# Kernel optimization log

Measured on AMD Instinct MI355X. Metric: run time of the kernel, lower is better.

Reference implementation:

```python
import jax, jax.numpy as jnp
import numpy as np

B, N, F = 8, 1024, 256
OUT, REL = 256, 16
NADJ = 7  # ((2 relations + consecutive) * 2 for backward) + self link


def setup_inputs() -> dict:
    key = jax.random.key(0)
    k0, k1, k2, k3, k4 = jax.random.split(key, 5)
    features = jax.random.normal(k0, (B, N, F), dtype=jnp.float32)
    A1 = jax.random.uniform(k1, (B, N, N), dtype=jnp.float32)
    A2 = jax.random.uniform(k2, (B, N, N), dtype=jnp.float32)
    # learned params: one (F+REL, OUT) weight per adjacency matrix, edge embeddings init 'ones', bias (N, OUT)
    W = jax.random.normal(k3, (NADJ, F + REL, OUT), dtype=jnp.float32) * 0.05
    W_edges = jnp.ones((NADJ, REL), dtype=jnp.float32)
    b = jax.random.uniform(k4, (N, OUT), dtype=jnp.float32, minval=-0.05, maxval=0.05)
    return {"features": features, "A1": A1, "A2": A2, "W": W, "W_edges": W_edges, "b": b}


def reference(features, A1, A2, W, W_edges, b):
    # eye = A[0] * zeros(N) + eye(N)  -> batch-broadcast identity [B,N,N]
    eye = jnp.zeros_like(A1) + jnp.eye(N, dtype=A1.dtype)
    # original rolls along axis 0 (batch) of the broadcast identity (faithful replication)
    shifted = jnp.roll(eye, 1, axis=0)
    A_fwd = [A1, A2, shifted]                      # relations + consecutive link
    A_list = A_fwd + [jnp.swapaxes(a, 1, 2) for a in A_fwd]  # backward links
    A_list.append(eye)                             # self links
    A = jnp.stack(A_list, axis=0)                  # [R,B,N,N]

    # concat(features, tile(W_edges[r])) @ W[r] == features @ W[r][:F] + W_edges[r] @ W[r][F:]
    HW = jnp.einsum('bnf,rfo->rbno', features, W[:, :F]) \
         + jnp.einsum('rd,rdo->ro', W_edges, W[:, F:])[:, None, None, :]  # [R,B,N,OUT]
    AHW = jnp.einsum('rbnm,rbmo->rbno', A, HW)     # batched adjacency matmul
    out = jnp.max(AHW, axis=0) + b                 # max-aggregate over relations, add bias
    return out                                     # activation = linear
```

## Files before the change

### kernel.cpp

```cpp
#include <hip/hip_runtime.h>
#include <hip/hip_bf16.h>

#define B_ 8
#define N_ 1024
#define F_ 256
#define OUT_ 256
#define REL_ 16
#define NADJ_ 7

typedef __attribute__((ext_vector_type(8))) _Float16 f16x8;
typedef __attribute__((ext_vector_type(4))) _Float16 f16x4;
typedef __attribute__((ext_vector_type(2))) _Float16 f16x2;
typedef __attribute__((ext_vector_type(4))) float f32x4;

__device__ __forceinline__ void gll16(const _Float16* g, _Float16* l) {
    __builtin_amdgcn_global_load_lds(
        (const __attribute__((address_space(1))) void*)g,
        (__attribute__((address_space(3))) void*)l, 16, 0, 0);
}

__device__ __forceinline__ f16x8 cvt8(float4 a, float4 b) {
    return f16x8{(_Float16)a.x, (_Float16)a.y, (_Float16)a.z, (_Float16)a.w,
                 (_Float16)b.x, (_Float16)b.y, (_Float16)b.z, (_Float16)b.w};
}

__constant__ const int c_perm[7] = {0, 1, 3, 4, 2, 5, 6};

__global__ __launch_bounds__(256) void prep_kernel(const float* __restrict__ W,
                                                   const float* __restrict__ We,
                                                   const float* __restrict__ feat,
                                                   float* __restrict__ cb,
                                                   _Float16* __restrict__ WTp,
                                                   _Float16* __restrict__ Fe) {
    int bid = blockIdx.x, tid = threadIdx.x;
    if (bid < 7) {
        int idx = bid * 256 + tid;
        int j = idx / OUT_, o = idx % OUT_;
        int r = c_perm[j];
        const float* Wr = W + (size_t)r * (F_ + REL_) * OUT_;
        float s = 0.f;
#pragma unroll
        for (int d = 0; d < REL_; ++d) s += We[r * REL_ + d] * Wr[(F_ + d) * OUT_ + o];
        cb[idx] = s;
    } else if (bid < 1799) {
        int idx = (bid - 7) * 256 + tid;
        int j = idx >> 16, rem = idx & 65535, o = rem >> 8, f = rem & 255;
        int r = c_perm[j];
        WTp[idx] = (_Float16)W[((size_t)r * (F_ + REL_) + f) * OUT_ + o];
    } else {
        int i = (bid - 1799) * 256 + tid;
        size_t base = (size_t)i * 8;
        float4 a = *(const float4*)(feat + base);
        float4 b = *(const float4*)(feat + base + 4);
        *(f16x8*)(Fe + base) = cvt8(a, b);
    }
}

__global__ __launch_bounds__(256) void hw7_kernel(const _Float16* __restrict__ Fe,
                                                  const _Float16* __restrict__ WTp,
                                                  const float* __restrict__ cb,
                                                  _Float16* __restrict__ HWT,
                                                  _Float16* __restrict__ HWN) {
    __shared__ _Float16 S[8192];
    const int bid = blockIdx.x, tid = threadIdx.x;
    const int z = bid / 128, rem = bid % 128, bx = rem & 63, by = rem >> 6;
    const bool tr = (z < 4);
    const _Float16* A  = tr ? (WTp + (size_t)z * 65536) : Fe;
    const _Float16* Bt = tr ? Fe : (WTp + (size_t)z * 65536);
    const int m0 = (tr ? by : bx) * 128;
    const int n0 = (tr ? bx : by) * 128;
    _Float16* As = S;
    _Float16* Bs = S + 4096;
    const int wave = tid >> 6, lane = tid & 63, lm = lane & 15, q = lane >> 4;
    const int wr = (wave >> 1) * 64, wc = (wave & 1) * 64;
    const int srow = tid >> 2, sk = (tid & 3) * 8;
    const _Float16* ga0 = A + (size_t)(m0 + srow) * F_ + sk;
    const _Float16* ga1 = ga0 + (size_t)64 * F_;
    const _Float16* gb0 = Bt + (size_t)(n0 + srow) * F_ + sk;
    const _Float16* gb1 = gb0 + (size_t)64 * F_;
    _Float16* la0 = As + tid * 8;
    _Float16* la1 = As + 2048 + tid * 8;
    _Float16* lb0 = Bs + tid * 8;
    _Float16* lb1 = Bs + 2048 + tid * 8;

    f32x4 acc[4][4] = {};
    for (int k0 = 0; k0 < F_; k0 += 32) {
        gll16(ga0 + k0, la0);
        gll16(ga1 + k0, la1);
        gll16(gb0 + k0, lb0);
        gll16(gb1 + k0, lb1);
        __syncthreads();
        f16x8 af[4], bf[4];
#pragma unroll
        for (int i = 0; i < 4; ++i) af[i] = *(const f16x8*)(As + (wr + i * 16 + lm) * 32 + q * 8);
#pragma unroll
        for (int j = 0; j < 4; ++j) bf[j] = *(const f16x8*)(Bs + (wc + j * 16 + lm) * 32 + q * 8);
#pragma unroll
        for (int i = 0; i < 4; ++i)
#pragma unroll
            for (int j = 0; j < 4; ++j)
                acc[i][j] = __builtin_amdgcn_mfma_f32_16x16x32_f16(af[i], bf[j], acc[i][j], 0, 0, 0);
        __syncthreads();
    }
    const float* cbz = cb + (size_t)z * 256;
    if (tr) {
        _Float16* C = HWT + (size_t)z * ((size_t)256 * 8192);
#pragma unroll
        for (int i = 0; i < 4; ++i)
#pragma unroll
            for (int j = 0; j < 4; ++j)
#pragma unroll
                for (int g = 0; g < 4; ++g) {
                    int row = wr + i * 16 + q * 4 + g;
                    int col = wc + j * 16 + lm;
                    float v = acc[i][j][g] + cbz[m0 + row];
                    C[(size_t)(m0 + row) * 8192 + (n0 + col)] = (_Float16)v;
                }
    } else {
        _Float16* C = HWN + (size_t)(z - 4) * ((size_t)8192 * 256);
#pragma unroll
        for (int i = 0; i < 4; ++i)
#pragma unroll
            for (int j = 0; j < 4; ++j)
#pragma unroll
                for (int g = 0; g < 4; ++g) {
                    int row = wr + i * 16 + q * 4 + g;
                    int col = wc + j * 16 + lm;
                    float v = acc[i][j][g] + cbz[n0 + col];
                    C[(size_t)(m0 + row) * 256 + (n0 + col)] = (_Float16)v;
                }
    }
}

__global__ __launch_bounds__(256) void p2_kernel(const float* __restrict__ A1,
                                                 const float* __restrict__ A2,
                                                 const _Float16* __restrict__ HWT,
                                                 _Float16* __restrict__ AHW) {
    __shared__ _Float16 As[2 * 4096];
    __shared__ _Float16 Bs[2 * 4096];
    const int d = blockIdx.x;
    const int xcd = d & 7, slot = d >> 3;
    const int Ghi = xcd + 8 * (slot >> 4);
    const int member = (slot >> 3) & 1;
    const int mt = slot & 7;
    const int kh = Ghi & 1;
    const int zz = Ghi >> 1;
    const int rr = zz >> 3, b = zz & 7;

    const size_t slab = (size_t)B_ * N_ * OUT_;
    const _Float16* Bt = HWT + (size_t)rr * (256 * 8192) + (size_t)b * 1024;
    _Float16* C = AHW + (size_t)kh * (4 * slab) + (size_t)rr * slab + (size_t)b * (N_ * OUT_);
    const int m0 = mt * 128, n0 = member * 128, kbase = kh * 512;
    const int tid = threadIdx.x;
    const int wave = tid >> 6, lane = tid & 63, lm = lane & 15, q = lane >> 4;
    const int wr = (wave >> 1) * 64, wc = (wave & 1) * 64;
    const int srow = tid >> 2, sk = (tid & 3) * 8;
    const _Float16* gb0 = Bt + (size_t)(n0 + srow) * 8192 + kbase + sk;
    const _Float16* gb1 = gb0 + (size_t)64 * 8192;
    _Float16* lb0 = Bs + tid * 8;
    _Float16* lb1 = Bs + 2048 + tid * 8;
    _Float16* la0 = As + srow * 32 + (((tid & 3) ^ ((tid >> 6) & 3)) * 8);

    const float* Ag = ((rr & 1) ? A2 : A1) + (size_t)b * N_ * N_;
    f32x4 acc[4][4] = {};

    auto domfma = [&]() {
#pragma unroll
        for (int u2 = 0; u2 < 2; ++u2) {
            const _Float16* Au = As + u2 * 4096;
            const _Float16* Bu = Bs + u2 * 4096;
            f16x8 af[4], bf[4];
#pragma unroll
            for (int i = 0; i < 4; ++i)
                af[i] = *(const f16x8*)(Au + (wr + i * 16 + lm) * 32 + ((q ^ i) * 8));
#pragma unroll
            for (int j = 0; j < 4; ++j)
                bf[j] = *(const f16x8*)(Bu + (wc + j * 16 + lm) * 32 + q * 8);
#pragma unroll
            for (int i = 0; i < 4; ++i)
#pragma unroll
                for (int j = 0; j < 4; ++j)
                    acc[i][j] = __builtin_amdgcn_mfma_f32_16x16x32_f16(af[i], bf[j], acc[i][j], 0, 0, 0);
        }
    };

    if (rr < 2) {
        const float* Ag0 = Ag + (size_t)(m0 + srow) * N_ + kbase + sk;
        const float* Ag1 = Ag0 + (size_t)64 * N_;
        float4 r0a = *(const float4*)(Ag0);
        float4 r0b = *(const float4*)(Ag0 + 4);
        float4 r1a = *(const float4*)(Ag0 + 32);
        float4 r1b = *(const float4*)(Ag0 + 36);
        float4 r2a = *(const float4*)(Ag1);
        float4 r2b = *(const float4*)(Ag1 + 4);
        float4 r3a = *(const float4*)(Ag1 + 32);
        float4 r3b = *(const float4*)(Ag1 + 36);
        for (int t = 0; t < 8; ++t) {
            gll16(gb0 + t * 64, lb0);
            gll16(gb0 + t * 64 + 32, lb0 + 4096);
            gll16(gb1 + t * 64, lb1);
            gll16(gb1 + t * 64 + 32, lb1 + 4096);
            *(f16x8*)(la0)        = cvt8(r0a, r0b);
            *(f16x8*)(la0 + 4096) = cvt8(r1a, r1b);
            *(f16x8*)(la0 + 2048) = cvt8(r2a, r2b);
            *(f16x8*)(la0 + 6144) = cvt8(r3a, r3b);
            if (t < 7) {
                const float* p0 = Ag0 + (t + 1) * 64;
                const float* p1 = Ag1 + (t + 1) * 64;
                r0a = *(const float4*)(p0);      r0b = *(const float4*)(p0 + 4);
                r1a = *(const float4*)(p0 + 32); r1b = *(const float4*)(p0 + 36);
                r2a = *(const float4*)(p1);      r2b = *(const float4*)(p1 + 4);
                r3a = *(const float4*)(p1 + 32); r3b = *(const float4*)(p1 + 36);
            }
            __syncthreads();
            domfma();
            __syncthreads();
        }
    } else {
        const int kk4 = (tid >> 4) * 4;
        const int ms = (tid & 15) * 8;
        const int u = kk4 >> 5, kl = kk4 & 31;
        const int tsw = ((ms >> 4) & 3) << 3;
        _Float16* wp = As + u * 4096 + ms * 32 + (kl ^ tsw);
        const float* gA = Ag + (size_t)(kbase + kk4) * N_ + m0 + ms;
        float4 ra0 = *(const float4*)(gA);
        float4 rb0 = *(const float4*)(gA + 4);
        float4 ra1 = *(const float4*)(gA + N_);
        float4 rb1 = *(const float4*)(gA + N_ + 4);
        float4 ra2 = *(const float4*)(gA + 2 * N_);
        float4 rb2 = *(const float4*)(gA + 2 * N_ + 4);
        float4 ra3 = *(const float4*)(gA + 3 * N_);
        float4 rb3 = *(const float4*)(gA + 3 * N_ + 4);
        for (int t = 0; t < 8; ++t) {
            gll16(gb0 + t * 64, lb0);
            gll16(gb0 + t * 64 + 32, lb0 + 4096);
            gll16(gb1 + t * 64, lb1);
            gll16(gb1 + t * 64 + 32, lb1 + 4096);
            *(f16x4*)(wp + 0 * 32) = f16x4{(_Float16)ra0.x, (_Float16)ra1.x, (_Float16)ra2.x, (_Float16)ra3.x};
            *(f16x4*)(wp + 1 * 32) = f16x4{(_Float16)ra0.y, (_Float16)ra1.y, (_Float16)ra2.y, (_Float16)ra3.y};
            *(f16x4*)(wp + 2 * 32) = f16x4{(_Float16)ra0.z, (_Float16)ra1.z, (_Float16)ra2.z, (_Float16)ra3.z};
            *(f16x4*)(wp + 3 * 32) = f16x4{(_Float16)ra0.w, (_Float16)ra1.w, (_Float16)ra2.w, (_Float16)ra3.w};
            *(f16x4*)(wp + 4 * 32) = f16x4{(_Float16)rb0.x, (_Float16)rb1.x, (_Float16)rb2.x, (_Float16)rb3.x};
            *(f16x4*)(wp + 5 * 32) = f16x4{(_Float16)rb0.y, (_Float16)rb1.y, (_Float16)rb2.y, (_Float16)rb3.y};
            *(f16x4*)(wp + 6 * 32) = f16x4{(_Float16)rb0.z, (_Float16)rb1.z, (_Float16)rb2.z, (_Float16)rb3.z};
            *(f16x4*)(wp + 7 * 32) = f16x4{(_Float16)rb0.w, (_Float16)rb1.w, (_Float16)rb2.w, (_Float16)rb3.w};
            if (t < 7) {
                const float* p = gA + (size_t)(t + 1) * 64 * N_;
                ra0 = *(const float4*)(p);          rb0 = *(const float4*)(p + 4);
                ra1 = *(const float4*)(p + N_);     rb1 = *(const float4*)(p + N_ + 4);
                ra2 = *(const float4*)(p + 2 * N_); rb2 = *(const float4*)(p + 2 * N_ + 4);
                ra3 = *(const float4*)(p + 3 * N_); rb3 = *(const float4*)(p + 3 * N_ + 4);
            }
            __syncthreads();
            domfma();
            __syncthreads();
        }
    }
#pragma unroll
    for (int i = 0; i < 4; ++i)
#pragma unroll
        for (int j = 0; j < 4; ++j)
#pragma unroll
            for (int g = 0; g < 4; ++g) {
                int row = wr + i * 16 + q * 4 + g;
                int col = wc + j * 16 + lm;
                C[(size_t)(m0 + row) * 256 + (n0 + col)] = (_Float16)acc[i][j][g];
            }
}

__global__ __launch_bounds__(256) void max_kernel(const _Float16* __restrict__ AHW,
                                                  const _Float16* __restrict__ HWN,
                                                  const float* __restrict__ bias,
                                                  float* __restrict__ out) {
    size_t i = ((size_t)blockIdx.x * 256 + threadIdx.x) * 8;
    const size_t slab = (size_t)B_ * N_ * OUT_;
    const size_t HS = 4 * slab;
    float m[8];
    {
        f16x8 v0 = *(const f16x8*)(AHW + i);
        f16x8 v1 = *(const f16x8*)(AHW + HS + i);
#pragma unroll
        for (int e = 0; e < 8; ++e) m[e] = (float)v0[e] + (float)v1[e];
    }
#pragma unroll
    for (int rr = 1; rr < 4; ++rr) {
        f16x8 v0 = *(const f16x8*)(AHW + rr * slab + i);
        f16x8 v1 = *(const f16x8*)(AHW + HS + rr * slab + i);
#pragma unroll
        for (int e = 0; e < 8; ++e) m[e] = fmaxf(m[e], (float)v0[e] + (float)v1[e]);
    }
#pragma unroll
    for (int j = 0; j < 3; ++j) {
        f16x8 w = *(const f16x8*)(HWN + j * slab + i);
#pragma unroll
        for (int e = 0; e < 8; ++e) m[e] = fmaxf(m[e], (float)w[e]);
    }
    size_t bidx = i & ((size_t)N_ * OUT_ - 1);
    float4 b0 = *(const float4*)(bias + bidx);
    float4 b1 = *(const float4*)(bias + bidx + 4);
    float4 o0 = {m[0] + b0.x, m[1] + b0.y, m[2] + b0.z, m[3] + b0.w};
    float4 o1 = {m[4] + b1.x, m[5] + b1.y, m[6] + b1.z, m[7] + b1.w};
    *(float4*)(out + i) = o0;
    *(float4*)(out + i + 4) = o1;
}

__global__ void cbias_kernel(const float* __restrict__ W, const float* __restrict__ We,
                             float* __restrict__ c) {
    int idx = blockIdx.x * 256 + threadIdx.x;
    if (idx >= NADJ_ * OUT_) return;
    int r = idx / OUT_, o = idx % OUT_;
    const float* Wr = W + (size_t)r * (F_ + REL_) * OUT_;
    float s = 0.f;
#pragma unroll
    for (int d = 0; d < REL_; ++d) s += We[r * REL_ + d] * Wr[(F_ + d) * OUT_ + o];
    c[idx] = s;
}

__global__ __launch_bounds__(256) void hw_kernel(const float* __restrict__ feat,
                                                 const float* __restrict__ W,
                                                 const float* __restrict__ cb,
                                                 _Float16* __restrict__ HWb) {
    __shared__ _Float16 As[64][32];
    __shared__ _Float16 Bs[64][32];
    const int mt = blockIdx.x, ct = blockIdx.y;
    const int tid = threadIdx.x, wave = tid >> 6, lane = tid & 63;
    const int r = (ct * 64) / OUT_;
    const int o0 = (ct * 64) % OUT_;
    const float* Bg = W + (size_t)r * (F_ + REL_) * OUT_ + o0;
    const int m0 = mt * 64;
    const int lm = lane & 15, q = lane >> 4;
    f32x4 acc[4] = {};
    for (int k0 = 0; k0 < F_; k0 += 32) {
        {
            int seg = (tid & 3) * 8, m = tid >> 2;
            const float* src = feat + (size_t)(m0 + m) * F_ + k0 + seg;
#pragma unroll
            for (int j = 0; j < 8; ++j) As[m][seg + j] = (_Float16)src[j];
        }
        {
            int kk = tid >> 3, ns = (tid & 7) * 8;
            const float* src = Bg + (size_t)(k0 + kk) * OUT_ + ns;
#pragma unroll
            for (int j = 0; j < 8; ++j) Bs[ns + j][kk] = (_Float16)src[j];
        }
        __syncthreads();
        f16x8 a = *(const f16x8*)&As[wave * 16 + lm][q * 8];
#pragma unroll
        for (int c4 = 0; c4 < 4; ++c4) {
            f16x8 b = *(const f16x8*)&Bs[c4 * 16 + lm][q * 8];
            acc[c4] = __builtin_amdgcn_mfma_f32_16x16x32_f16(a, b, acc[c4], 0, 0, 0);
        }
        __syncthreads();
    }
#pragma unroll
    for (int c4 = 0; c4 < 4; ++c4)
#pragma unroll
        for (int g = 0; g < 4; ++g) {
            int row = wave * 16 + (lane >> 4) * 4 + g;
            int col = c4 * 16 + lm;
            float v = acc[c4][g] + cb[r * OUT_ + o0 + col];
            HWb[((size_t)r * B_ * N_ + m0 + row) * OUT_ + o0 + col] = (_Float16)v;
        }
}

__global__ __launch_bounds__(256) void agg_kernel(const float* __restrict__ A1,
                                                  const float* __restrict__ A2,
                                                  const _Float16* __restrict__ HWb,
                                                  const float* __restrict__ bias,
                                                  float* __restrict__ out) {
    __shared__ _Float16 As[64][32];
    __shared__ _Float16 Bs[64][32];
    const int b = blockIdx.z, nt = blockIdx.y, ot = blockIdx.x;
    const int tid = threadIdx.x, wave = tid >> 6, lane = tid & 63;
    const int n0 = nt * 64, o0 = ot * 64;
    const int lm = lane & 15, q = lane >> 4;
    const size_t rstride = (size_t)B_ * N_ * OUT_;
    f32x4 mx[4];
#pragma unroll
    for (int i = 0; i < 4; ++i) mx[i] = f32x4{-1e30f, -1e30f, -1e30f, -1e30f};
#pragma unroll 1
    for (int rr = 0; rr < 4; ++rr) {
        const float* Ag = ((rr & 1) ? A2 : A1) + (size_t)b * N_ * N_;
        const bool tr = (rr >= 2);
        const int r = (rr < 2) ? rr : rr + 1;
        const _Float16* Bg = HWb + (size_t)r * rstride + (size_t)b * N_ * OUT_ + o0;
        f32x4 acc[4] = {};
        for (int k0 = 0; k0 < N_; k0 += 32) {
            if (!tr) {
                int seg = (tid & 3) * 8, m = tid >> 2;
                const float* src = Ag + (size_t)(n0 + m) * N_ + k0 + seg;
#pragma unroll
                for (int j = 0; j < 8; ++j) As[m][seg + j] = (_Float16)src[j];
            } else {
                int kk = tid >> 3, ms = (tid & 7) * 8;
                const float* src = Ag + (size_t)(k0 + kk) * N_ + n0 + ms;
#pragma unroll
                for (int j = 0; j < 8; ++j) As[ms + j][kk] = (_Float16)src[j];
            }
            {
                int kk = tid >> 3, ns = (tid & 7) * 8;
                const _Float16* src = Bg + (size_t)(k0 + kk) * OUT_ + ns;
#pragma unroll
                for (int j = 0; j < 8; ++j) Bs[ns + j][kk] = src[j];
            }
            __syncthreads();
            f16x8 a = *(const f16x8*)&As[wave * 16 + lm][q * 8];
#pragma unroll
            for (int c4 = 0; c4 < 4; ++c4) {
                f16x8 bb = *(const f16x8*)&Bs[c4 * 16 + lm][q * 8];
                acc[c4] = __builtin_amdgcn_mfma_f32_16x16x32_f16(a, bb, acc[c4], 0, 0, 0);
            }
            __syncthreads();
        }
#pragma unroll
        for (int c4 = 0; c4 < 4; ++c4)
#pragma unroll
            for (int g = 0; g < 4; ++g) mx[c4][g] = fmaxf(mx[c4][g], acc[c4][g]);
    }
#pragma unroll
    for (int c4 = 0; c4 < 4; ++c4)
#pragma unroll
        for (int g = 0; g < 4; ++g) {
            int row = wave * 16 + (lane >> 4) * 4 + g;
            int col = c4 * 16 + lm;
            size_t pos = ((size_t)b * N_ + n0 + row) * OUT_ + o0 + col;
            float v = mx[c4][g];
            v = fmaxf(v, (float)HWb[2 * rstride + pos]);
            v = fmaxf(v, (float)HWb[5 * rstride + pos]);
            v = fmaxf(v, (float)HWb[6 * rstride + pos]);
            out[pos] = v + bias[((size_t)(n0 + row)) * OUT_ + o0 + col];
        }
}

extern "C" void kernel_launch(void* const* d_in, const int* in_sizes, int n_in,
                              void* d_out, int out_size, void* d_ws, size_t ws_size,
                              hipStream_t stream) {
    const float* feat = (const float*)d_in[0];
    const float* A1   = (const float*)d_in[1];
    const float* A2   = (const float*)d_in[2];
    const float* W    = (const float*)d_in[3];
    const float* We   = (const float*)d_in[4];
    const float* bias = (const float*)d_in[5];
    float* out = (float*)d_out;

    const size_t OFF_CB   = 0;
    const size_t OFF_WT   = 8192;
    const size_t OFF_FE   = 1048576;
    const size_t OFF_HWT  = 5242880;
    const size_t OFF_HWN  = 22020096;
    const size_t OFF_AHW  = 34603008;
    const size_t WS_NEEDED = 68157440;

    if (ws_size >= WS_NEEDED) {
        float*    cbp = (float*)((char*)d_ws + OFF_CB);
        _Float16* WTp = (_Float16*)((char*)d_ws + OFF_WT);
        _Float16* Fe  = (_Float16*)((char*)d_ws + OFF_FE);
        _Float16* HWT = (_Float16*)((char*)d_ws + OFF_HWT);
        _Float16* HWN = (_Float16*)((char*)d_ws + OFF_HWN);
        _Float16* AHW = (_Float16*)((char*)d_ws + OFF_AHW);

        prep_kernel<<<2823, 256, 0, stream>>>(W, We, feat, cbp, WTp, Fe);
        hw7_kernel<<<896, 256, 0, stream>>>(Fe, WTp, cbp, HWT, HWN);
        p2_kernel<<<1024, 256, 0, stream>>>(A1, A2, HWT, AHW);
        max_kernel<<<1024, 256, 0, stream>>>(AHW, HWN, bias, out);
    } else {
        float* cb = (float*)d_ws;
        _Float16* HWb = (_Float16*)((char*)d_ws + 8192);
        cbias_kernel<<<7, 256, 0, stream>>>(W, We, cb);
        hw_kernel<<<dim3(128, 28), 256, 0, stream>>>(feat, W, cb, HWb);
        agg_kernel<<<dim3(4, 16, 8), 256, 0, stream>>>(A1, A2, HWb, bias, out);
    }
}
```

Baseline: 174.5 us.

## Double-buffer LDS in GEMM kernels and fuse max over direct relations

```diff
diff --git a/kernel.cpp b/kernel.cpp
--- a/kernel.cpp
+++ b/kernel.cpp
@@ -10,7 +10,6 @@
 
 typedef __attribute__((ext_vector_type(8))) _Float16 f16x8;
 typedef __attribute__((ext_vector_type(4))) _Float16 f16x4;
-typedef __attribute__((ext_vector_type(2))) _Float16 f16x2;
 typedef __attribute__((ext_vector_type(4))) float f32x4;
 
 __device__ __forceinline__ void gll16(const _Float16* g, _Float16* l) {
@@ -60,50 +59,57 @@
                                                   const _Float16* __restrict__ WTp,
                                                   const float* __restrict__ cb,
                                                   _Float16* __restrict__ HWT,
-                                                  _Float16* __restrict__ HWN) {
-    __shared__ _Float16 S[8192];
+                                                  _Float16* __restrict__ HWNm) {
+    __shared__ _Float16 S[2 * 8192];
     const int bid = blockIdx.x, tid = threadIdx.x;
-    const int z = bid / 128, rem = bid % 128, bx = rem & 63, by = rem >> 6;
-    const bool tr = (z < 4);
-    const _Float16* A  = tr ? (WTp + (size_t)z * 65536) : Fe;
-    const _Float16* Bt = tr ? Fe : (WTp + (size_t)z * 65536);
-    const int m0 = (tr ? by : bx) * 128;
-    const int n0 = (tr ? bx : by) * 128;
-    _Float16* As = S;
-    _Float16* Bs = S + 4096;
     const int wave = tid >> 6, lane = tid & 63, lm = lane & 15, q = lane >> 4;
     const int wr = (wave >> 1) * 64, wc = (wave & 1) * 64;
     const int srow = tid >> 2, sk = (tid & 3) * 8;
-    const _Float16* ga0 = A + (size_t)(m0 + srow) * F_ + sk;
-    const _Float16* ga1 = ga0 + (size_t)64 * F_;
-    const _Float16* gb0 = Bt + (size_t)(n0 + srow) * F_ + sk;
-    const _Float16* gb1 = gb0 + (size_t)64 * F_;
-    _Float16* la0 = As + tid * 8;
-    _Float16* la1 = As + 2048 + tid * 8;
-    _Float16* lb0 = Bs + tid * 8;
-    _Float16* lb1 = Bs + 2048 + tid * 8;
 
     f32x4 acc[4][4] = {};
-    for (int k0 = 0; k0 < F_; k0 += 32) {
-        gll16(ga0 + k0, la0);
-        gll16(ga1 + k0, la1);
-        gll16(gb0 + k0, lb0);
-        gll16(gb1 + k0, lb1);
-        __syncthreads();
+
+    auto mfma_step = [&](const _Float16* Au, const _Float16* Bu) {
         f16x8 af[4], bf[4];
 #pragma unroll
-        for (int i = 0; i < 4; ++i) af[i] = *(const f16x8*)(As + (wr + i * 16 + lm) * 32 + q * 8);
-#pragma unroll
-        for (int j = 0; j < 4; ++j) bf[j] = *(const f16x8*)(Bs + (wc + j * 16 + lm) * 32 + q * 8);
+        for (int i = 0; i < 4; ++i) af[i] = *(const f16x8*)(Au + (wr + i * 16 + lm) * 32 + q * 8);
+#pragma unroll
+        for (int j = 0; j < 4; ++j) bf[j] = *(const f16x8*)(Bu + (wc + j * 16 + lm) * 32 + q * 8);
 #pragma unroll
         for (int i = 0; i < 4; ++i)
 #pragma unroll
             for (int j = 0; j < 4; ++j)
                 acc[i][j] = __builtin_amdgcn_mfma_f32_16x16x32_f16(af[i], bf[j], acc[i][j], 0, 0, 0);
+    };
+
+    if (bid < 512) {
+        const int z = bid >> 7, rem = bid & 127, bx = rem & 63, by = rem >> 6;
+        const _Float16* A  = WTp + (size_t)z * 65536;
+        const _Float16* Bt = Fe;
+        const int m0 = by * 128;
+        const int n0 = bx * 128;
+        const _Float16* ga0 = A + (size_t)(m0 + srow) * F_ + sk;
+        const _Float16* ga1 = ga0 + (size_t)64 * F_;
+        const _Float16* gb0 = Bt + (size_t)(n0 + srow) * F_ + sk;
+        const _Float16* gb1 = gb0 + (size_t)64 * F_;
+        gll16(ga0, S + tid * 8);
+        gll16(ga1, S + 2048 + tid * 8);
+        gll16(gb0, S + 4096 + tid * 8);
+        gll16(gb1, S + 6144 + tid * 8);
         __syncthreads();
-    }
-    const float* cbz = cb + (size_t)z * 256;
-    if (tr) {
+        for (int t = 0; t < 8; ++t) {
+            const int c = t & 1, n = c ^ 1;
+            if (t < 7) {
+                const int k = (t + 1) * 32;
+                _Float16* base = S + n * 8192;
+                gll16(ga0 + k, base + tid * 8);
+                gll16(ga1 + k, base + 2048 + tid * 8);
+                gll16(gb0 + k, base + 4096 + tid * 8);
+                gll16(gb1 + k, base + 6144 + tid * 8);
+            }
+            mfma_step(S + c * 8192, S + c * 8192 + 4096);
+            __syncthreads();
+        }
+        const float* cbz = cb + (size_t)z * 256;
         _Float16* C = HWT + (size_t)z * ((size_t)256 * 8192);
 #pragma unroll
         for (int i = 0; i < 4; ++i)
@@ -117,7 +123,55 @@
                     C[(size_t)(m0 + row) * 8192 + (n0 + col)] = (_Float16)v;
                 }
     } else {
-        _Float16* C = HWN + (size_t)(z - 4) * ((size_t)8192 * 256);
+        const int idx = bid - 512, bx = idx & 63, by = idx >> 6;
+        const int m0 = bx * 128;
+        const int n0 = by * 128;
+        const _Float16* ga0 = Fe + (size_t)(m0 + srow) * F_ + sk;
+        const _Float16* ga1 = ga0 + (size_t)64 * F_;
+        float mx[4][4][4];
+#pragma unroll
+        for (int i = 0; i < 4; ++i)
+#pragma unroll
+            for (int j = 0; j < 4; ++j)
+#pragma unroll
+                for (int g = 0; g < 4; ++g) mx[i][j][g] = -1e30f;
+#pragma unroll 1
+        for (int zi = 4; zi < 7; ++zi) {
+            const _Float16* gb0 = WTp + (size_t)zi * 65536 + (size_t)(n0 + srow) * F_ + sk;
+            const _Float16* gb1 = gb0 + (size_t)64 * F_;
+#pragma unroll
+            for (int i = 0; i < 4; ++i)
+#pragma unroll
+                for (int j = 0; j < 4; ++j) acc[i][j] = f32x4{0.f, 0.f, 0.f, 0.f};
+            gll16(ga0, S + tid * 8);
+            gll16(ga1, S + 2048 + tid * 8);
+            gll16(gb0, S + 4096 + tid * 8);
+            gll16(gb1, S + 6144 + tid * 8);
+            __syncthreads();
+            for (int t = 0; t < 8; ++t) {
+                const int c = t & 1, n = c ^ 1;
+                if (t < 7) {
+                    const int k = (t + 1) * 32;
+                    _Float16* base = S + n * 8192;
+                    gll16(ga0 + k, base + tid * 8);
+                    gll16(ga1 + k, base + 2048 + tid * 8);
+                    gll16(gb0 + k, base + 4096 + tid * 8);
+                    gll16(gb1 + k, base + 6144 + tid * 8);
+                }
+                mfma_step(S + c * 8192, S + c * 8192 + 4096);
+                __syncthreads();
+            }
+            const float* cbz = cb + (size_t)zi * 256;
+#pragma unroll
+            for (int i = 0; i < 4; ++i)
+#pragma unroll
+                for (int j = 0; j < 4; ++j)
+#pragma unroll
+                    for (int g = 0; g < 4; ++g) {
+                        int col = wc + j * 16 + lm;
+                        mx[i][j][g] = fmaxf(mx[i][j][g], acc[i][j][g] + cbz[n0 + col]);
+                    }
+        }
 #pragma unroll
         for (int i = 0; i < 4; ++i)
 #pragma unroll
@@ -126,8 +180,7 @@
                 for (int g = 0; g < 4; ++g) {
                     int row = wr + i * 16 + q * 4 + g;
                     int col = wc + j * 16 + lm;
-                    float v = acc[i][j][g] + cbz[n0 + col];
-                    C[(size_t)(m0 + row) * 256 + (n0 + col)] = (_Float16)v;
+                    HWNm[(size_t)(m0 + row) * 256 + (n0 + col)] = (_Float16)mx[i][j][g];
                 }
     }
 }
@@ -157,102 +210,105 @@
     const int srow = tid >> 2, sk = (tid & 3) * 8;
     const _Float16* gb0 = Bt + (size_t)(n0 + srow) * 8192 + kbase + sk;
     const _Float16* gb1 = gb0 + (size_t)64 * 8192;
-    _Float16* lb0 = Bs + tid * 8;
-    _Float16* lb1 = Bs + 2048 + tid * 8;
-    _Float16* la0 = As + srow * 32 + (((tid & 3) ^ ((tid >> 6) & 3)) * 8);
 
     const float* Ag = ((rr & 1) ? A2 : A1) + (size_t)b * N_ * N_;
     f32x4 acc[4][4] = {};
 
-    auto domfma = [&]() {
-#pragma unroll
-        for (int u2 = 0; u2 < 2; ++u2) {
-            const _Float16* Au = As + u2 * 4096;
-            const _Float16* Bu = Bs + u2 * 4096;
-            f16x8 af[4], bf[4];
-#pragma unroll
-            for (int i = 0; i < 4; ++i)
-                af[i] = *(const f16x8*)(Au + (wr + i * 16 + lm) * 32 + ((q ^ i) * 8));
+    auto mfma_step = [&](int c) {
+        const _Float16* Au = As + c * 4096;
+        const _Float16* Bu = Bs + c * 4096;
+        f16x8 af[4], bf[4];
+#pragma unroll
+        for (int i = 0; i < 4; ++i)
+            af[i] = *(const f16x8*)(Au + (wr + i * 16 + lm) * 32 + ((q ^ i) * 8));
+#pragma unroll
+        for (int j = 0; j < 4; ++j)
+            bf[j] = *(const f16x8*)(Bu + (wc + j * 16 + lm) * 32 + q * 8);
+#pragma unroll
+        for (int i = 0; i < 4; ++i)
 #pragma unroll
             for (int j = 0; j < 4; ++j)
-                bf[j] = *(const f16x8*)(Bu + (wc + j * 16 + lm) * 32 + q * 8);
-#pragma unroll
-            for (int i = 0; i < 4; ++i)
-#pragma unroll
-                for (int j = 0; j < 4; ++j)
-                    acc[i][j] = __builtin_amdgcn_mfma_f32_16x16x32_f16(af[i], bf[j], acc[i][j], 0, 0, 0);
-        }
+                acc[i][j] = __builtin_amdgcn_mfma_f32_16x16x32_f16(af[i], bf[j], acc[i][j], 0, 0, 0);
     };
 
     if (rr < 2) {
         const float* Ag0 = Ag + (size_t)(m0 + srow) * N_ + kbase + sk;
         const float* Ag1 = Ag0 + (size_t)64 * N_;
-        float4 r0a = *(const float4*)(Ag0);
-        float4 r0b = *(const float4*)(Ag0 + 4);
-        float4 r1a = *(const float4*)(Ag0 + 32);
-        float4 r1b = *(const float4*)(Ag0 + 36);
-        float4 r2a = *(const float4*)(Ag1);
-        float4 r2b = *(const float4*)(Ag1 + 4);
-        float4 r3a = *(const float4*)(Ag1 + 32);
-        float4 r3b = *(const float4*)(Ag1 + 36);
-        for (int t = 0; t < 8; ++t) {
-            gll16(gb0 + t * 64, lb0);
-            gll16(gb0 + t * 64 + 32, lb0 + 4096);
-            gll16(gb1 + t * 64, lb1);
-            gll16(gb1 + t * 64 + 32, lb1 + 4096);
-            *(f16x8*)(la0)        = cvt8(r0a, r0b);
-            *(f16x8*)(la0 + 4096) = cvt8(r1a, r1b);
-            *(f16x8*)(la0 + 2048) = cvt8(r2a, r2b);
-            *(f16x8*)(la0 + 6144) = cvt8(r3a, r3b);
-            if (t < 7) {
-                const float* p0 = Ag0 + (t + 1) * 64;
-                const float* p1 = Ag1 + (t + 1) * 64;
-                r0a = *(const float4*)(p0);      r0b = *(const float4*)(p0 + 4);
-                r1a = *(const float4*)(p0 + 32); r1b = *(const float4*)(p0 + 36);
-                r2a = *(const float4*)(p1);      r2b = *(const float4*)(p1 + 4);
-                r3a = *(const float4*)(p1 + 32); r3b = *(const float4*)(p1 + 36);
-            }
+        const int sx = ((tid & 3) ^ ((tid >> 6) & 3)) * 8;
+        float4 pa = *(const float4*)(Ag0);
+        float4 pb = *(const float4*)(Ag0 + 4);
+        float4 pc = *(const float4*)(Ag1);
+        float4 pd = *(const float4*)(Ag1 + 4);
+        *(f16x8*)(As + srow * 32 + sx) = cvt8(pa, pb);
+        *(f16x8*)(As + 2048 + srow * 32 + sx) = cvt8(pc, pd);
+        gll16(gb0, Bs + tid * 8);
+        gll16(gb1, Bs + 2048 + tid * 8);
+        pa = *(const float4*)(Ag0 + 32); pb = *(const float4*)(Ag0 + 36);
+        pc = *(const float4*)(Ag1 + 32); pd = *(const float4*)(Ag1 + 36);
+        __syncthreads();
+        for (int t = 0; t < 16; ++t) {
+            const int c = t & 1, n = c ^ 1;
+            if (t < 15) {
+                _Float16* la = As + n * 4096 + srow * 32 + sx;
+                *(f16x8*)(la) = cvt8(pa, pb);
+                *(f16x8*)(la + 2048) = cvt8(pc, pd);
+                gll16(gb0 + (t + 1) * 32, Bs + n * 4096 + tid * 8);
+                gll16(gb1 + (t + 1) * 32, Bs + n * 4096 + 2048 + tid * 8);
+                if (t < 14) {
+                    const int k = (t + 2) * 32;
+                    pa = *(const float4*)(Ag0 + k); pb = *(const float4*)(Ag0 + k + 4);
+                    pc = *(const float4*)(Ag1 + k); pd = *(const float4*)(Ag1 + k + 4);
+                }
+            }
+            mfma_step(c);
             __syncthreads();
-            domfma();
-            __syncthreads();
         }
     } else {
-        const int kk4 = (tid >> 4) * 4;
-        const int ms = (tid & 15) * 8;
-        const int u = kk4 >> 5, kl = kk4 & 31;
-        const int tsw = ((ms >> 4) & 3) << 3;
-        _Float16* wp = As + u * 4096 + ms * 32 + (kl ^ tsw);
-        const float* gA = Ag + (size_t)(kbase + kk4) * N_ + m0 + ms;
+        const int kk4 = (tid >> 5) * 4;
+        const int ms4 = (tid & 31) * 4;
+        const int tsw = ((ms4 >> 4) & 3) << 3;
+        const int wof = ms4 * 32 + (kk4 ^ tsw);
+        const float* gA = Ag + (size_t)(kbase + kk4) * N_ + m0 + ms4;
         float4 ra0 = *(const float4*)(gA);
-        float4 rb0 = *(const float4*)(gA + 4);
         float4 ra1 = *(const float4*)(gA + N_);
-        float4 rb1 = *(const float4*)(gA + N_ + 4);
         float4 ra2 = *(const float4*)(gA + 2 * N_);
-        float4 rb2 = *(const float4*)(gA + 2 * N_ + 4);
         float4 ra3 = *(const float4*)(gA + 3 * N_);
-        float4 rb3 = *(const float4*)(gA + 3 * N_ + 4);
-        for (int t = 0; t < 8; ++t) {
-            gll16(gb0 + t * 64, lb0);
-            gll16(gb0 + t * 64 + 32, lb0 + 4096);
-            gll16(gb1 + t * 64, lb1);
-            gll16(gb1 + t * 64 + 32, lb1 + 4096);
+        {
+            _Float16* wp = As + wof;
             *(f16x4*)(wp + 0 * 32) = f16x4{(_Float16)ra0.x, (_Float16)ra1.x, (_Float16)ra2.x, (_Float16)ra3.x};
             *(f16x4*)(wp + 1 * 32) = f16x4{(_Float16)ra0.y, (_Float16)ra1.y, (_Float16)ra2.y, (_Float16)ra3.y};
             *(f16x4*)(wp + 2 * 32) = f16x4{(_Float16)ra0.z, (_Float16)ra1.z, (_Float16)ra2.z, (_Float16)ra3.z};
             *(f16x4*)(wp + 3 * 32) = f16x4{(_Float16)ra0.w, (_Float16)ra1.w, (_Float16)ra2.w, (_Float16)ra3.w};
-            *(f16x4*)(wp + 4 * 32) = f16x4{(_Float16)rb0.x, (_Float16)rb1.x, (_Float16)rb2.x, (_Float16)rb3.x};
-            *(f16x4*)(wp + 5 * 32) = f16x4{(_Float16)rb0.y, (_Float16)rb1.y, (_Float16)rb2.y, (_Float16)rb3.y};
-            *(f16x4*)(wp + 6 * 32) = f16x4{(_Float16)rb0.z, (_Float16)rb1.z, (_Float16)rb2.z, (_Float16)rb3.z};
-            *(f16x4*)(wp + 7 * 32) = f16x4{(_Float16)rb0.w, (_Float16)rb1.w, (_Float16)rb2.w, (_Float16)rb3.w};
-            if (t < 7) {
-                const float* p = gA + (size_t)(t + 1) * 64 * N_;
-                ra0 = *(const float4*)(p);          rb0 = *(const float4*)(p + 4);
-                ra1 = *(const float4*)(p + N_);     rb1 = *(const float4*)(p + N_ + 4);
-                ra2 = *(const float4*)(p + 2 * N_); rb2 = *(const float4*)(p + 2 * N_ + 4);
-                ra3 = *(const float4*)(p + 3 * N_); rb3 = *(const float4*)(p + 3 * N_ + 4);
-            }
-            __syncthreads();
-            domfma();
+        }
+        gll16(gb0, Bs + tid * 8);
+        gll16(gb1, Bs + 2048 + tid * 8);
+        {
+            const float* p = gA + (size_t)32 * N_;
+            ra0 = *(const float4*)(p);
+            ra1 = *(const float4*)(p + N_);
+            ra2 = *(const float4*)(p + 2 * N_);
+            ra3 = *(const float4*)(p + 3 * N_);
+        }
+        __syncthreads();
+        for (int t = 0; t < 16; ++t) {
+            const int c = t & 1, n = c ^ 1;
+            if (t < 15) {
+                _Float16* wp = As + n * 4096 + wof;
+                *(f16x4*)(wp + 0 * 32) = f16x4{(_Float16)ra0.x, (_Float16)ra1.x, (_Float16)ra2.x, (_Float16)ra3.x};
+                *(f16x4*)(wp + 1 * 32) = f16x4{(_Float16)ra0.y, (_Float16)ra1.y, (_Float16)ra2.y, (_Float16)ra3.y};
+                *(f16x4*)(wp + 2 * 32) = f16x4{(_Float16)ra0.z, (_Float16)ra1.z, (_Float16)ra2.z, (_Float16)ra3.z};
+                *(f16x4*)(wp + 3 * 32) = f16x4{(_Float16)ra0.w, (_Float16)ra1.w, (_Float16)ra2.w, (_Float16)ra3.w};
+                gll16(gb0 + (t + 1) * 32, Bs + n * 4096 + tid * 8);
+                gll16(gb1 + (t + 1) * 32, Bs + n * 4096 + 2048 + tid * 8);
+                if (t < 14) {
+                    const float* p = gA + (size_t)(t + 2) * 32 * N_;
+                    ra0 = *(const float4*)(p);
+                    ra1 = *(const float4*)(p + N_);
+                    ra2 = *(const float4*)(p + 2 * N_);
+                    ra3 = *(const float4*)(p + 3 * N_);
+                }
+            }
+            mfma_step(c);
             __syncthreads();
         }
     }
@@ -269,7 +325,7 @@
 }
 
 __global__ __launch_bounds__(256) void max_kernel(const _Float16* __restrict__ AHW,
-                                                  const _Float16* __restrict__ HWN,
+                                                  const _Float16* __restrict__ HWNm,
                                                   const float* __restrict__ bias,
                                                   float* __restrict__ out) {
     size_t i = ((size_t)blockIdx.x * 256 + threadIdx.x) * 8;
@@ -289,9 +345,8 @@
 #pragma unroll
         for (int e = 0; e < 8; ++e) m[e] = fmaxf(m[e], (float)v0[e] + (float)v1[e]);
     }
-#pragma unroll
-    for (int j = 0; j < 3; ++j) {
-        f16x8 w = *(const f16x8*)(HWN + j * slab + i);
+    {
+        f16x8 w = *(const f16x8*)(HWNm + i);
 #pragma unroll
         for (int e = 0; e < 8; ++e) m[e] = fmaxf(m[e], (float)w[e]);
     }
@@ -447,22 +502,22 @@
     const size_t OFF_WT   = 8192;
     const size_t OFF_FE   = 1048576;
     const size_t OFF_HWT  = 5242880;
-    const size_t OFF_HWN  = 22020096;
-    const size_t OFF_AHW  = 34603008;
-    const size_t WS_NEEDED = 68157440;
+    const size_t OFF_HWNM = 22020096;
+    const size_t OFF_AHW  = 26214400;
+    const size_t WS_NEEDED = 59768832;
 
     if (ws_size >= WS_NEEDED) {
-        float*    cbp = (float*)((char*)d_ws + OFF_CB);
-        _Float16* WTp = (_Float16*)((char*)d_ws + OFF_WT);
-        _Float16* Fe  = (_Float16*)((char*)d_ws + OFF_FE);
-        _Float16* HWT = (_Float16*)((char*)d_ws + OFF_HWT);
-        _Float16* HWN = (_Float16*)((char*)d_ws + OFF_HWN);
-        _Float16* AHW = (_Float16*)((char*)d_ws + OFF_AHW);
+        float*    cbp  = (float*)((char*)d_ws + OFF_CB);
+        _Float16* WTp  = (_Float16*)((char*)d_ws + OFF_WT);
+        _Float16* Fe   = (_Float16*)((char*)d_ws + OFF_FE);
+        _Float16* HWT  = (_Float16*)((char*)d_ws + OFF_HWT);
+        _Float16* HWNm = (_Float16*)((char*)d_ws + OFF_HWNM);
+        _Float16* AHW  = (_Float16*)((char*)d_ws + OFF_AHW);
 
         prep_kernel<<<2823, 256, 0, stream>>>(W, We, feat, cbp, WTp, Fe);
-        hw7_kernel<<<896, 256, 0, stream>>>(Fe, WTp, cbp, HWT, HWN);
+        hw7_kernel<<<640, 256, 0, stream>>>(Fe, WTp, cbp, HWT, HWNm);
         p2_kernel<<<1024, 256, 0, stream>>>(A1, A2, HWT, AHW);
-        max_kernel<<<1024, 256, 0, stream>>>(AHW, HWN, bias, out);
+        max_kernel<<<1024, 256, 0, stream>>>(AHW, HWNm, bias, out);
     } else {
         float* cb = (float*)d_ws;
         _Float16* HWb = (_Float16*)((char*)d_ws + 8192);
```

Result: slower. 182.6 us (+4.6%).

## Multi-buffer LDS staging in HW and adjacency GEMMs, relayout HWT per batch

Applied to the files above, without the earlier changes.

```diff
diff --git a/kernel.cpp b/kernel.cpp
--- a/kernel.cpp
+++ b/kernel.cpp
@@ -10,7 +10,6 @@
 
 typedef __attribute__((ext_vector_type(8))) _Float16 f16x8;
 typedef __attribute__((ext_vector_type(4))) _Float16 f16x4;
-typedef __attribute__((ext_vector_type(2))) _Float16 f16x2;
 typedef __attribute__((ext_vector_type(4))) float f32x4;
 
 __device__ __forceinline__ void gll16(const _Float16* g, _Float16* l) {
@@ -23,6 +22,8 @@
     return f16x8{(_Float16)a.x, (_Float16)a.y, (_Float16)a.z, (_Float16)a.w,
                  (_Float16)b.x, (_Float16)b.y, (_Float16)b.z, (_Float16)b.w};
 }
+
+#define MEMPIN() asm volatile("" ::: "memory")
 
 __constant__ const int c_perm[7] = {0, 1, 3, 4, 2, 5, 6};
 
@@ -61,7 +62,7 @@
                                                   const float* __restrict__ cb,
                                                   _Float16* __restrict__ HWT,
                                                   _Float16* __restrict__ HWN) {
-    __shared__ _Float16 S[8192];
+    __shared__ _Float16 S[3 * 8192];
     const int bid = blockIdx.x, tid = threadIdx.x;
     const int z = bid / 128, rem = bid % 128, bx = rem & 63, by = rem >> 6;
     const bool tr = (z < 4);
@@ -69,8 +70,6 @@
     const _Float16* Bt = tr ? Fe : (WTp + (size_t)z * 65536);
     const int m0 = (tr ? by : bx) * 128;
     const int n0 = (tr ? bx : by) * 128;
-    _Float16* As = S;
-    _Float16* Bs = S + 4096;
     const int wave = tid >> 6, lane = tid & 63, lm = lane & 15, q = lane >> 4;
     const int wr = (wave >> 1) * 64, wc = (wave & 1) * 64;
     const int srow = tid >> 2, sk = (tid & 3) * 8;
@@ -78,33 +77,60 @@
     const _Float16* ga1 = ga0 + (size_t)64 * F_;
     const _Float16* gb0 = Bt + (size_t)(n0 + srow) * F_ + sk;
     const _Float16* gb1 = gb0 + (size_t)64 * F_;
-    _Float16* la0 = As + tid * 8;
-    _Float16* la1 = As + 2048 + tid * 8;
-    _Float16* lb0 = Bs + tid * 8;
-    _Float16* lb1 = Bs + 2048 + tid * 8;
 
     f32x4 acc[4][4] = {};
-    for (int k0 = 0; k0 < F_; k0 += 32) {
-        gll16(ga0 + k0, la0);
-        gll16(ga1 + k0, la1);
-        gll16(gb0 + k0, lb0);
-        gll16(gb1 + k0, lb1);
-        __syncthreads();
-        f16x8 af[4], bf[4];
-#pragma unroll
-        for (int i = 0; i < 4; ++i) af[i] = *(const f16x8*)(As + (wr + i * 16 + lm) * 32 + q * 8);
-#pragma unroll
-        for (int j = 0; j < 4; ++j) bf[j] = *(const f16x8*)(Bs + (wc + j * 16 + lm) * 32 + q * 8);
-#pragma unroll
-        for (int i = 0; i < 4; ++i)
-#pragma unroll
-            for (int j = 0; j < 4; ++j)
-                acc[i][j] = __builtin_amdgcn_mfma_f32_16x16x32_f16(af[i], bf[j], acc[i][j], 0, 0, 0);
-        __syncthreads();
+    const int NT = 8;
+
+    {
+        gll16(ga0, S + tid * 8);
+        gll16(ga1, S + 2048 + tid * 8);
+        gll16(gb0, S + 4096 + tid * 8);
+        gll16(gb1, S + 6144 + tid * 8);
+        MEMPIN();
+        gll16(ga0 + 32, S + 8192 + tid * 8);
+        gll16(ga1 + 32, S + 8192 + 2048 + tid * 8);
+        gll16(gb0 + 32, S + 8192 + 4096 + tid * 8);
+        gll16(gb1 + 32, S + 8192 + 6144 + tid * 8);
+        asm volatile("s_waitcnt vmcnt(4)" ::: "memory");
+        __builtin_amdgcn_s_barrier();
+    }
+    int cs = 0, ns = 1, fs = 2;
+    for (int t = 0; t < NT; ++t) {
+        if (t + 2 < NT) {
+            const int k = (t + 2) * 32;
+            _Float16* sb = S + fs * 8192;
+            gll16(ga0 + k, sb + tid * 8);
+            gll16(ga1 + k, sb + 2048 + tid * 8);
+            gll16(gb0 + k, sb + 4096 + tid * 8);
+            gll16(gb1 + k, sb + 6144 + tid * 8);
+        }
+        {
+            const _Float16* Au = S + cs * 8192;
+            const _Float16* Bu = Au + 4096;
+            f16x8 af[4], bf[4];
+#pragma unroll
+            for (int i = 0; i < 4; ++i) af[i] = *(const f16x8*)(Au + (wr + i * 16 + lm) * 32 + q * 8);
+#pragma unroll
+            for (int j = 0; j < 4; ++j) bf[j] = *(const f16x8*)(Bu + (wc + j * 16 + lm) * 32 + q * 8);
+            __builtin_amdgcn_s_setprio(1);
+#pragma unroll
+            for (int i = 0; i < 4; ++i)
+#pragma unroll
+                for (int j = 0; j < 4; ++j)
+                    acc[i][j] = __builtin_amdgcn_mfma_f32_16x16x32_f16(af[i], bf[j], acc[i][j], 0, 0, 0);
+            __builtin_amdgcn_s_setprio(0);
+        }
+        if (t + 1 < NT) {
+            if (t + 2 < NT) asm volatile("s_waitcnt vmcnt(4)" ::: "memory");
+            else            asm volatile("s_waitcnt vmcnt(0)" ::: "memory");
+            __builtin_amdgcn_s_barrier();
+        }
+        int tmp = cs; cs = ns; ns = fs; fs = tmp;
     }
     const float* cbz = cb + (size_t)z * 256;
     if (tr) {
-        _Float16* C = HWT + (size_t)z * ((size_t)256 * 8192);
+        _Float16* C = HWT + (size_t)z * (8 * 256 * 1024) + (size_t)(n0 >> 10) * (256 * 1024);
+        const int nl = n0 & 1023;
 #pragma unroll
         for (int i = 0; i < 4; ++i)
 #pragma unroll
@@ -114,7 +140,7 @@
                     int row = wr + i * 16 + q * 4 + g;
                     int col = wc + j * 16 + lm;
                     float v = acc[i][j][g] + cbz[m0 + row];
-                    C[(size_t)(m0 + row) * 8192 + (n0 + col)] = (_Float16)v;
+                    C[(size_t)(m0 + row) * 1024 + nl + col] = (_Float16)v;
                 }
     } else {
         _Float16* C = HWN + (size_t)(z - 4) * ((size_t)8192 * 256);
@@ -136,8 +162,8 @@
                                                  const float* __restrict__ A2,
                                                  const _Float16* __restrict__ HWT,
                                                  _Float16* __restrict__ AHW) {
-    __shared__ _Float16 As[2 * 4096];
-    __shared__ _Float16 Bs[2 * 4096];
+    __shared__ _Float16 As[2 * 8192];
+    __shared__ _Float16 Bs[2 * 8192];
     const int d = blockIdx.x;
     const int xcd = d & 7, slot = d >> 3;
     const int Ghi = xcd + 8 * (slot >> 4);
@@ -148,27 +174,24 @@
     const int rr = zz >> 3, b = zz & 7;
 
     const size_t slab = (size_t)B_ * N_ * OUT_;
-    const _Float16* Bt = HWT + (size_t)rr * (256 * 8192) + (size_t)b * 1024;
+    const _Float16* Bt = HWT + (size_t)(rr * 8 + b) * (256 * 1024);
     _Float16* C = AHW + (size_t)kh * (4 * slab) + (size_t)rr * slab + (size_t)b * (N_ * OUT_);
     const int m0 = mt * 128, n0 = member * 128, kbase = kh * 512;
     const int tid = threadIdx.x;
     const int wave = tid >> 6, lane = tid & 63, lm = lane & 15, q = lane >> 4;
     const int wr = (wave >> 1) * 64, wc = (wave & 1) * 64;
     const int srow = tid >> 2, sk = (tid & 3) * 8;
-    const _Float16* gb0 = Bt + (size_t)(n0 + srow) * 8192 + kbase + sk;
-    const _Float16* gb1 = gb0 + (size_t)64 * 8192;
-    _Float16* lb0 = Bs + tid * 8;
-    _Float16* lb1 = Bs + 2048 + tid * 8;
-    _Float16* la0 = As + srow * 32 + (((tid & 3) ^ ((tid >> 6) & 3)) * 8);
+    const _Float16* gb0 = Bt + (size_t)(n0 + srow) * 1024 + kbase + sk;
+    const _Float16* gb1 = gb0 + (size_t)64 * 1024;
 
     const float* Ag = ((rr & 1) ? A2 : A1) + (size_t)b * N_ * N_;
     f32x4 acc[4][4] = {};
 
-    auto domfma = [&]() {
+    auto domfma = [&](int buf) {
 #pragma unroll
         for (int u2 = 0; u2 < 2; ++u2) {
-            const _Float16* Au = As + u2 * 4096;
-            const _Float16* Bu = Bs + u2 * 4096;
+            const _Float16* Au = As + buf * 8192 + u2 * 4096;
+            const _Float16* Bu = Bs + buf * 8192 + u2 * 4096;
             f16x8 af[4], bf[4];
 #pragma unroll
             for (int i = 0; i < 4; ++i)
@@ -176,44 +199,55 @@
 #pragma unroll
             for (int j = 0; j < 4; ++j)
                 bf[j] = *(const f16x8*)(Bu + (wc + j * 16 + lm) * 32 + q * 8);
+            __builtin_amdgcn_s_setprio(1);
 #pragma unroll
             for (int i = 0; i < 4; ++i)
 #pragma unroll
                 for (int j = 0; j < 4; ++j)
                     acc[i][j] = __builtin_amdgcn_mfma_f32_16x16x32_f16(af[i], bf[j], acc[i][j], 0, 0, 0);
-        }
+            __builtin_amdgcn_s_setprio(0);
+        }
+    };
+
+    auto stageB = [&](int buf, int k2) {
+        _Float16* base = Bs + buf * 8192;
+        gll16(gb0 + k2,      base + tid * 8);
+        gll16(gb0 + k2 + 32, base + 4096 + tid * 8);
+        gll16(gb1 + k2,      base + 2048 + tid * 8);
+        gll16(gb1 + k2 + 32, base + 6144 + tid * 8);
     };
 
     if (rr < 2) {
         const float* Ag0 = Ag + (size_t)(m0 + srow) * N_ + kbase + sk;
         const float* Ag1 = Ag0 + (size_t)64 * N_;
-        float4 r0a = *(const float4*)(Ag0);
-        float4 r0b = *(const float4*)(Ag0 + 4);
-        float4 r1a = *(const float4*)(Ag0 + 32);
-        float4 r1b = *(const float4*)(Ag0 + 36);
-        float4 r2a = *(const float4*)(Ag1);
-        float4 r2b = *(const float4*)(Ag1 + 4);
-        float4 r3a = *(const float4*)(Ag1 + 32);
-        float4 r3b = *(const float4*)(Ag1 + 36);
+        const int sx = ((tid & 3) ^ ((tid >> 6) & 3)) * 8;
+        float4 r0a, r0b, r1a, r1b, r2a, r2b, r3a, r3b;
+        auto RDA = [&](int k2) {
+            r0a = *(const float4*)(Ag0 + k2);      r0b = *(const float4*)(Ag0 + k2 + 4);
+            r1a = *(const float4*)(Ag0 + k2 + 32); r1b = *(const float4*)(Ag0 + k2 + 36);
+            r2a = *(const float4*)(Ag1 + k2);      r2b = *(const float4*)(Ag1 + k2 + 4);
+            r3a = *(const float4*)(Ag1 + k2 + 32); r3b = *(const float4*)(Ag1 + k2 + 36);
+        };
+        auto WRA = [&](int buf) {
+            _Float16* la = As + buf * 8192 + srow * 32 + sx;
+            *(f16x8*)(la)        = cvt8(r0a, r0b);
+            *(f16x8*)(la + 4096) = cvt8(r1a, r1b);
+            *(f16x8*)(la + 2048) = cvt8(r2a, r2b);
+            *(f16x8*)(la + 6144) = cvt8(r3a, r3b);
+        };
+        RDA(0);
+        WRA(0);
+        stageB(0, 0);
+        RDA(64);
+        __syncthreads();
         for (int t = 0; t < 8; ++t) {
-            gll16(gb0 + t * 64, lb0);
-            gll16(gb0 + t * 64 + 32, lb0 + 4096);
-            gll16(gb1 + t * 64, lb1);
-            gll16(gb1 + t * 64 + 32, lb1 + 4096);
-            *(f16x8*)(la0)        = cvt8(r0a, r0b);
-            *(f16x8*)(la0 + 4096) = cvt8(r1a, r1b);
-            *(f16x8*)(la0 + 2048) = cvt8(r2a, r2b);
-            *(f16x8*)(la0 + 6144) = cvt8(r3a, r3b);
+            const int cur = t & 1, nxt = cur ^ 1;
             if (t < 7) {
-                const float* p0 = Ag0 + (t + 1) * 64;
-                const float* p1 = Ag1 + (t + 1) * 64;
-                r0a = *(const float4*)(p0);      r0b = *(const float4*)(p0 + 4);
-                r1a = *(const float4*)(p0 + 32); r1b = *(const float4*)(p0 + 36);
-                r2a = *(const float4*)(p1);      r2b = *(const float4*)(p1 + 4);
-                r3a = *(const float4*)(p1 + 32); r3b = *(const float4*)(p1 + 36);
+                WRA(nxt);
+                stageB(nxt, (t + 1) * 64);
+                if (t < 6) RDA((t + 2) * 64);
             }
-            __syncthreads();
-            domfma();
+            domfma(cur);
             __syncthreads();
         }
     } else {
@@ -221,21 +255,18 @@
         const int ms = (tid & 15) * 8;
         const int u = kk4 >> 5, kl = kk4 & 31;
         const int tsw = ((ms >> 4) & 3) << 3;
-        _Float16* wp = As + u * 4096 + ms * 32 + (kl ^ tsw);
+        const int wof = u * 4096 + ms * 32 + (kl ^ tsw);
         const float* gA = Ag + (size_t)(kbase + kk4) * N_ + m0 + ms;
-        float4 ra0 = *(const float4*)(gA);
-        float4 rb0 = *(const float4*)(gA + 4);
-        float4 ra1 = *(const float4*)(gA + N_);
-        float4 rb1 = *(const float4*)(gA + N_ + 4);
-        float4 ra2 = *(const float4*)(gA + 2 * N_);
-        float4 rb2 = *(const float4*)(gA + 2 * N_ + 4);
-        float4 ra3 = *(const float4*)(gA + 3 * N_);
-        float4 rb3 = *(const float4*)(gA + 3 * N_ + 4);
-        for (int t = 0; t < 8; ++t) {
-            gll16(gb0 + t * 64, lb0);
-            gll16(gb0 + t * 64 + 32, lb0 + 4096);
-            gll16(gb1 + t * 64, lb1);
-            gll16(gb1 + t * 64 + 32, lb1 + 4096);
+        float4 ra0, rb0, ra1, rb1, ra2, rb2, ra3, rb3;
+        auto RDT = [&](int t) {
+            const float* p = gA + (size_t)t * 64 * N_;
+            ra0 = *(const float4*)(p);            rb0 = *(const float4*)(p + 4);
+            ra1 = *(const float4*)(p + N_);       rb1 = *(const float4*)(p + N_ + 4);
+            ra2 = *(const float4*)(p + 2 * N_);   rb2 = *(const float4*)(p + 2 * N_ + 4);
+            ra3 = *(const float4*)(p + 3 * N_);   rb3 = *(const float4*)(p + 3 * N_ + 4);
+        };
+        auto WRT = [&](int buf) {
+            _Float16* wp = As + buf * 8192 + wof;
             *(f16x4*)(wp + 0 * 32) = f16x4{(_Float16)ra0.x, (_Float16)ra1.x, (_Float16)ra2.x, (_Float16)ra3.x};
             *(f16x4*)(wp + 1 * 32) = f16x4{(_Float16)ra0.y, (_Float16)ra1.y, (_Float16)ra2.y, (_Float16)ra3.y};
             *(f16x4*)(wp + 2 * 32) = f16x4{(_Float16)ra0.z, (_Float16)ra1.z, (_Float16)ra2.z, (_Float16)ra3.z};
@@ -244,15 +275,20 @@
             *(f16x4*)(wp + 5 * 32) = f16x4{(_Float16)rb0.y, (_Float16)rb1.y, (_Float16)rb2.y, (_Float16)rb3.y};
             *(f16x4*)(wp + 6 * 32) = f16x4{(_Float16)rb0.z, (_Float16)rb1.z, (_Float16)rb2.z, (_Float16)rb3.z};
             *(f16x4*)(wp + 7 * 32) = f16x4{(_Float16)rb0.w, (_Float16)rb1.w, (_Float16)rb2.w, (_Float16)rb3.w};
+        };
+        RDT(0);
+        WRT(0);
+        stageB(0, 0);
+        RDT(1);
+        __syncthreads();
+        for (int t = 0; t < 8; ++t) {
+            const int cur = t & 1, nxt = cur ^ 1;
             if (t < 7) {
-                const float* p = gA + (size_t)(t + 1) * 64 * N_;
-                ra0 = *(const float4*)(p);          rb0 = *(const float4*)(p + 4);
-                ra1 = *(const float4*)(p + N_);     rb1 = *(const float4*)(p + N_ + 4);
-                ra2 = *(const float4*)(p + 2 * N_); rb2 = *(const float4*)(p + 2 * N_ + 4);
-                ra3 = *(const float4*)(p + 3 * N_); rb3 = *(const float4*)(p + 3 * N_ + 4);
+                WRT(nxt);
+                stageB(nxt, (t + 1) * 64);
+                if (t < 6) RDT(t + 2);
             }
-            __syncthreads();
-            domfma();
+            domfma(cur);
             __syncthreads();
         }
     }
```

After: 167.5 us. 4.0% less time.
